# Optimization experiments

Measured on AMD Instinct MI355X. Metric: run time of the kernel, lower is better.

## Reference

```python
import jax, jax.numpy as jnp
import numpy as np

BATCH = 4096
N_CTRL = 64      # num_control_points
ORDER = 3        # spline degree p
DIM = 3          # spatial dimension (channels = DIM + 1, last is weight)
OUT_DIM = 2048   # sampled points per curve


def _gen_knot_vector(order, num_control_points, delta=1e-06):
    m = order + num_control_points + 1
    num_segments = m - 2 * (order + 1) + 1
    kv = [(j + 1) * delta for j in range(order)]
    kv += list(np.linspace(delta * (order + 1), 1.0, num_segments + 1))
    kv += [1.0 for _ in range(order)]
    return np.asarray(kv, dtype=np.float64)


def _find_span(n, p, u, U):
    # n = num_ctrl - 1; returns span index in [p, n]
    if u >= U[n + 1]:
        return n
    if u <= U[p]:
        return p
    low, high = p, n + 1
    mid = (low + high) // 2
    while u < U[mid] or u >= U[mid + 1]:
        if u < U[mid]:
            high = mid
        else:
            low = mid
        mid = (low + high) // 2
    return mid


def _basis_funs(span, u, p, U):
    # Cox-de Boor recursion (NURBS book A2.2) -> p+1 nonzero basis values
    N = np.zeros(p + 1)
    N[0] = 1.0
    left = np.zeros(p + 1)
    right = np.zeros(p + 1)
    for j in range(1, p + 1):
        left[j] = u - U[span + 1 - j]
        right[j] = U[span + j] - u
        saved = 0.0
        for r in range(j):
            temp = N[r] / (right[r + 1] + left[j - r])
            N[r] = saved + right[r + 1] * temp
            saved = left[j - r] * temp
        N[j] = saved
    return N


def _precompute_basis():
    U = _gen_knot_vector(ORDER, N_CTRL)
    u_params = np.linspace(0.0, 1.0, OUT_DIM)
    n = N_CTRL - 1
    spans = np.empty(OUT_DIM, dtype=np.int32)
    basis = np.empty((OUT_DIM, ORDER + 1), dtype=np.float32)
    for i, u in enumerate(u_params):
        s = _find_span(n, ORDER, u, U)
        spans[i] = s
        basis[i] = _basis_funs(s, u, ORDER, U)
    return spans, basis


def setup_inputs() -> dict:
    key = jax.random.key(0)
    k_xyz, k_w = jax.random.split(key)
    xyz = jax.random.normal(k_xyz, (BATCH, N_CTRL, DIM), dtype=jnp.float32)
    # positive rational weights to keep the homogeneous divide well-conditioned
    w = jax.random.uniform(k_w, (BATCH, N_CTRL, 1), dtype=jnp.float32) + 0.5
    control_points = jnp.concatenate([xyz, w], axis=-1)  # [B, N, DIM+1]
    spans_np, basis_np = _precompute_basis()
    return {
        "control_points": control_points,
        "span": jnp.asarray(spans_np),          # [S] int32, values in [ORDER, N_CTRL-1]
        "basis": jnp.asarray(basis_np),         # [S, ORDER+1] float32
    }


def reference(control_points, span, basis):
    p = basis.shape[1] - 1
    dim = control_points.shape[-1] - 1
    # curves[b, s, :] = sum_j basis[s, j] * control_points[b, span[s] - p + j, :]
    curves = basis[:, 0][None, :, None] * control_points[:, span - p, :]
    for j in range(1, p + 1):
        curves = curves + basis[:, j][None, :, None] * control_points[:, span - p + j, :]
    # rational (homogeneous) divide
    return curves[:, :, :dim] / curves[:, :, dim][:, :, None]
```

## Files before the change

kernel.cpp:

```cpp
#include <hip/hip_runtime.h>

#define BATCH  4096
#define NCTRL  64
#define SDIM   2048
#define WSZ    64
#define VPT    4
#define CHUNK  (WSZ * VPT)
#define NCHUNK 4
#define NXCD   8

__global__ __launch_bounds__(WSZ, 8) void curve_eval_kernel(
    const float4* __restrict__ cp,
    const int*    __restrict__ span,
    const float4* __restrict__ basis,
    float4*       __restrict__ out)
{
    __shared__ float4 cp_s[NCTRL + 1];
    __shared__ float4 out_s4[CHUNK * 3 / 4];

    const int wg   = blockIdx.x;
    const int x    = wg & (NXCD - 1);
    const int i    = wg >> 3;
    const int b    = x * (BATCH / NXCD) + (i >> 1);
    const int s0b  = (i & 1) * (CHUNK * NCHUNK);
    const int tid  = threadIdx.x;

    const float4 cpv = cp[(size_t)b * NCTRL + tid];
    cp_s[tid] = cpv;
    if (tid == NCTRL - 1) cp_s[NCTRL] = cpv;
    __syncthreads();

    for (int c = 0; c < NCHUNK; ++c) {
        const int s0 = s0b + c * CHUNK;

        const int  sbase = s0 + tid * VPT;
        const int4 sp4   = reinterpret_cast<const int4*>(span)[(s0 >> 2) + tid];
        const int  sp0   = sp4.x;
        const int  spk[VPT] = {sp4.x, sp4.y, sp4.z, sp4.w};

        float4 rows[5];
        #pragma unroll
        for (int j = 0; j < 5; ++j) rows[j] = cp_s[sp0 - 3 + j];

        float o[VPT * 3];
        #pragma unroll
        for (int k = 0; k < VPT; ++k) {
            const float4 bas = basis[sbase + k];
            const bool hi = (spk[k] > sp0);
            const float w0 = hi ? 0.0f  : bas.x;
            const float w1 = hi ? bas.x : bas.y;
            const float w2 = hi ? bas.y : bas.z;
            const float w3 = hi ? bas.z : bas.w;
            const float w4 = hi ? bas.w : 0.0f;

            const float xx = w0*rows[0].x + w1*rows[1].x + w2*rows[2].x + w3*rows[3].x + w4*rows[4].x;
            const float yy = w0*rows[0].y + w1*rows[1].y + w2*rows[2].y + w3*rows[3].y + w4*rows[4].y;
            const float zz = w0*rows[0].z + w1*rows[1].z + w2*rows[2].z + w3*rows[3].z + w4*rows[4].z;
            const float ww = w0*rows[0].w + w1*rows[1].w + w2*rows[2].w + w3*rows[3].w + w4*rows[4].w;

            const float invw = __builtin_amdgcn_rcpf(ww);
            o[k * 3 + 0] = xx * invw;
            o[k * 3 + 1] = yy * invw;
            o[k * 3 + 2] = zz * invw;
        }

        float4* mine = &out_s4[tid * 3];
        mine[0] = make_float4(o[0], o[1],  o[2],  o[3]);
        mine[1] = make_float4(o[4], o[5],  o[6],  o[7]);
        mine[2] = make_float4(o[8], o[9],  o[10], o[11]);
        __syncthreads();

        const size_t base4 = ((size_t)b * SDIM + (size_t)s0) * 3u / 4u;
        #pragma unroll
        for (int k = 0; k < 3; ++k) {
            out[base4 + tid + k * WSZ] = out_s4[tid + k * WSZ];
        }
    }
}

extern "C" void kernel_launch(void* const* d_in, const int* in_sizes, int n_in,
                              void* d_out, int out_size, void* d_ws, size_t ws_size,
                              hipStream_t stream) {
    const float4* cp    = (const float4*)d_in[0];
    const int*    span  = (const int*)d_in[1];
    const float4* basis = (const float4*)d_in[2];
    float4*       out   = (float4*)d_out;

    const int nblocks = BATCH * SDIM / (CHUNK * NCHUNK);
    curve_eval_kernel<<<nblocks, WSZ, 0, stream>>>(cp, span, basis, out);
}
```

Before: 27.24 us.

## Split serial chunk loop across four waves per block with per-wave staging

Replaces the single-wave block that looped over four output chunks with a 256-thread block in which each wave handles one chunk concurrently. Each wave gets its own LDS staging region and uses a wave-local lgkmcnt wait instead of a block barrier before the coalesced store. This trades serial per-wave latency for more parallel waves per control-point load. Only one wave loads the control points, and larger blocks may change occupancy.

```diff
diff --git a/kernel.cpp b/kernel.cpp
--- a/kernel.cpp
+++ b/kernel.cpp
@@ -3,78 +3,82 @@
 #define BATCH  4096
 #define NCTRL  64
 #define SDIM   2048
+#define BLK    256
 #define WSZ    64
+#define NWAVE  (BLK / WSZ)
 #define VPT    4
 #define CHUNK  (WSZ * VPT)
-#define NCHUNK 4
 #define NXCD   8
 
-__global__ __launch_bounds__(WSZ, 8) void curve_eval_kernel(
+__global__ __launch_bounds__(BLK, 8) void curve_eval_kernel(
     const float4* __restrict__ cp,
     const int*    __restrict__ span,
     const float4* __restrict__ basis,
     float4*       __restrict__ out)
 {
     __shared__ float4 cp_s[NCTRL + 1];
-    __shared__ float4 out_s4[CHUNK * 3 / 4];
+    __shared__ float4 out_s4[NWAVE * CHUNK * 3 / 4];
 
     const int wg   = blockIdx.x;
     const int x    = wg & (NXCD - 1);
     const int i    = wg >> 3;
     const int b    = x * (BATCH / NXCD) + (i >> 1);
-    const int s0b  = (i & 1) * (CHUNK * NCHUNK);
+    const int s0b  = (i & 1) * (NWAVE * CHUNK);
     const int tid  = threadIdx.x;
+    const int wid  = tid >> 6;
+    const int lane = tid & (WSZ - 1);
 
-    const float4 cpv = cp[(size_t)b * NCTRL + tid];
-    cp_s[tid] = cpv;
-    if (tid == NCTRL - 1) cp_s[NCTRL] = cpv;
+    if (tid < NCTRL) {
+        const float4 cpv = cp[(size_t)b * NCTRL + tid];
+        cp_s[tid] = cpv;
+        if (tid == NCTRL - 1) cp_s[NCTRL] = cpv;
+    }
     __syncthreads();
 
-    for (int c = 0; c < NCHUNK; ++c) {
-        const int s0 = s0b + c * CHUNK;
+    const int s0    = s0b + wid * CHUNK;
+    const int sbase = s0 + lane * VPT;
+    const int4 sp4  = reinterpret_cast<const int4*>(span)[(s0 >> 2) + lane];
+    const int  sp0  = sp4.x;
+    const int  spk[VPT] = {sp4.x, sp4.y, sp4.z, sp4.w};
 
-        const int  sbase = s0 + tid * VPT;
-        const int4 sp4   = reinterpret_cast<const int4*>(span)[(s0 >> 2) + tid];
-        const int  sp0   = sp4.x;
-        const int  spk[VPT] = {sp4.x, sp4.y, sp4.z, sp4.w};
+    float4 rows[5];
+    #pragma unroll
+    for (int j = 0; j < 5; ++j) rows[j] = cp_s[sp0 - 3 + j];
 
-        float4 rows[5];
-        #pragma unroll
-        for (int j = 0; j < 5; ++j) rows[j] = cp_s[sp0 - 3 + j];
+    float o[VPT * 3];
+    #pragma unroll
+    for (int k = 0; k < VPT; ++k) {
+        const float4 bas = basis[sbase + k];
+        const bool hi = (spk[k] > sp0);
+        const float w0 = hi ? 0.0f  : bas.x;
+        const float w1 = hi ? bas.x : bas.y;
+        const float w2 = hi ? bas.y : bas.z;
+        const float w3 = hi ? bas.z : bas.w;
+        const float w4 = hi ? bas.w : 0.0f;
 
-        float o[VPT * 3];
-        #pragma unroll
-        for (int k = 0; k < VPT; ++k) {
-            const float4 bas = basis[sbase + k];
-            const bool hi = (spk[k] > sp0);
-            const float w0 = hi ? 0.0f  : bas.x;
-            const float w1 = hi ? bas.x : bas.y;
-            const float w2 = hi ? bas.y : bas.z;
-            const float w3 = hi ? bas.z : bas.w;
-            const float w4 = hi ? bas.w : 0.0f;
+        const float xx = w0*rows[0].x + w1*rows[1].x + w2*rows[2].x + w3*rows[3].x + w4*rows[4].x;
+        const float yy = w0*rows[0].y + w1*rows[1].y + w2*rows[2].y + w3*rows[3].y + w4*rows[4].y;
+        const float zz = w0*rows[0].z + w1*rows[1].z + w2*rows[2].z + w3*rows[3].z + w4*rows[4].z;
+        const float ww = w0*rows[0].w + w1*rows[1].w + w2*rows[2].w + w3*rows[3].w + w4*rows[4].w;
 
-            const float xx = w0*rows[0].x + w1*rows[1].x + w2*rows[2].x + w3*rows[3].x + w4*rows[4].x;
-            const float yy = w0*rows[0].y + w1*rows[1].y + w2*rows[2].y + w3*rows[3].y + w4*rows[4].y;
-            const float zz = w0*rows[0].z + w1*rows[1].z + w2*rows[2].z + w3*rows[3].z + w4*rows[4].z;
-            const float ww = w0*rows[0].w + w1*rows[1].w + w2*rows[2].w + w3*rows[3].w + w4*rows[4].w;
+        const float invw = __builtin_amdgcn_rcpf(ww);
+        o[k * 3 + 0] = xx * invw;
+        o[k * 3 + 1] = yy * invw;
+        o[k * 3 + 2] = zz * invw;
+    }
 
-            const float invw = __builtin_amdgcn_rcpf(ww);
-            o[k * 3 + 0] = xx * invw;
-            o[k * 3 + 1] = yy * invw;
-            o[k * 3 + 2] = zz * invw;
-        }
+    float4* region = &out_s4[wid * (CHUNK * 3 / 4)];
+    float4* mine   = &region[lane * 3];
+    mine[0] = make_float4(o[0], o[1],  o[2],  o[3]);
+    mine[1] = make_float4(o[4], o[5],  o[6],  o[7]);
+    mine[2] = make_float4(o[8], o[9],  o[10], o[11]);
 
-        float4* mine = &out_s4[tid * 3];
-        mine[0] = make_float4(o[0], o[1],  o[2],  o[3]);
-        mine[1] = make_float4(o[4], o[5],  o[6],  o[7]);
-        mine[2] = make_float4(o[8], o[9],  o[10], o[11]);
-        __syncthreads();
+    asm volatile("s_waitcnt lgkmcnt(0)" ::: "memory");
 
-        const size_t base4 = ((size_t)b * SDIM + (size_t)s0) * 3u / 4u;
-        #pragma unroll
-        for (int k = 0; k < 3; ++k) {
-            out[base4 + tid + k * WSZ] = out_s4[tid + k * WSZ];
-        }
+    const size_t base4 = ((size_t)b * SDIM + (size_t)s0) * 3u / 4u;
+    #pragma unroll
+    for (int k = 0; k < 3; ++k) {
+        out[base4 + lane + k * WSZ] = region[lane + k * WSZ];
     }
 }
 
@@ -86,6 +90,6 @@
     const float4* basis = (const float4*)d_in[2];
     float4*       out   = (float4*)d_out;
 
-    const int nblocks = BATCH * SDIM / (CHUNK * NCHUNK);
-    curve_eval_kernel<<<nblocks, WSZ, 0, stream>>>(cp, span, basis, out);
+    const int nblocks = BATCH * SDIM / (NWAVE * CHUNK);
+    curve_eval_kernel<<<nblocks, BLK, 0, stream>>>(cp, span, basis, out);
 }
```

New measurement: 24.21 us. -11.1%, faster.
